# Optimization experiments

Measured on AMD Instinct MI355X. Metric: run time of the kernel, lower is better.

## Reference

```python
import jax, jax.numpy as jnp
import numpy as np

N, E = 50000, 800000
IN_DIM, HID, ZDIM = 256, 128, 64
LN_EPS = 1e-5


def _layernorm(x, gamma, beta):
    mu = jnp.mean(x, axis=-1, keepdims=True)
    var = jnp.mean(jnp.square(x - mu), axis=-1, keepdims=True)
    return (x - mu) * jax.lax.rsqrt(var + LN_EPS) * gamma + beta


def _gcn_conv(h, src, dst, dinv, W, b):
    # h: (N, d_in) -> (N, d_out). GCNConv: X W, then sym-normalized
    # aggregation over edges with self-loops, then bias.
    h = h @ W                                   # (N, d_out)
    coef = dinv[src] * dinv[dst]                # (E,)
    agg = jax.ops.segment_sum(h[src] * coef[:, None], dst,
                              num_segments=h.shape[0])
    agg = agg + h * jnp.square(dinv)[:, None]   # self-loop term
    return agg + b


def setup_inputs() -> dict:
    key = jax.random.key(0)
    ks = jax.random.split(key, 5)
    x = jax.random.normal(ks[0], (N, IN_DIM), dtype=jnp.float32)
    edge_index = jax.random.randint(ks[1], (2, E), 0, N, dtype=jnp.int64)
    s1 = 1.0 / np.sqrt(IN_DIM)
    s2 = 1.0 / np.sqrt(HID)
    return {
        "x": x,
        "edge_index": edge_index,
        "ln_gamma": jnp.ones((IN_DIM,), jnp.float32),
        "ln_beta": jnp.zeros((IN_DIM,), jnp.float32),
        "W1": jax.random.normal(ks[2], (IN_DIM, HID), jnp.float32) * s1,
        "b1": jnp.zeros((HID,), jnp.float32),
        "W2": jax.random.normal(ks[3], (HID, HID), jnp.float32) * s2,
        "b2": jnp.zeros((HID,), jnp.float32),
        "W3": jax.random.normal(ks[4], (HID, ZDIM), jnp.float32) * s2,
        "b3": jnp.zeros((ZDIM,), jnp.float32),
    }


def reference(x, edge_index, ln_gamma, ln_beta, W1, b1, W2, b2, W3, b3):
    src, dst = edge_index[0], edge_index[1]
    n = x.shape[0]
    # degree with self-loops (dropout is inference no-op, training=False)
    deg = jnp.ones((n,), x.dtype).at[dst].add(1.0)
    dinv = jax.lax.rsqrt(deg)
    h = _layernorm(x, ln_gamma, ln_beta)
    h = jax.nn.relu(_gcn_conv(h, src, dst, dinv, W1, b1))
    h = jax.nn.relu(_gcn_conv(h, src, dst, dinv, W2, b2))
    z = _gcn_conv(h, src, dst, dinv, W3, b3)
    return z
```

## Files before the change

kernel.cpp:

```cpp
#include <hip/hip_runtime.h>
#include <cstdint>
#include <cstddef>


typedef __attribute__((ext_vector_type(8))) __bf16 bf16x8;
typedef __attribute__((ext_vector_type(4))) float f32x4;
typedef _Float16 half_t;
typedef __attribute__((ext_vector_type(8))) _Float16 half8_t;

__global__ __launch_bounds__(256) void prep_misc(
    const float* __restrict__ x, const float* __restrict__ W1,
    const float* __restrict__ W2, const float* __restrict__ W3,
    int* __restrict__ bcnt, int* __restrict__ bcur_zero,
    unsigned short* __restrict__ W1t_hi, unsigned short* __restrict__ W1t_lo,
    unsigned short* __restrict__ W2t_hi, unsigned short* __restrict__ W2t_lo,
    unsigned short* __restrict__ W3t_hi, unsigned short* __restrict__ W3t_lo,
    float* __restrict__ mu, float* __restrict__ rs, int n) {
  int blk = blockIdx.x;
  int tid = threadIdx.x;
  if (blk == 0) {
    bcnt[tid] = 0;
    bcur_zero[tid] = 0;
    return;
  }
  if (blk <= 224) {
    int idx = (blk - 1) * 256 + tid;
    const float* W;
    unsigned short *Th, *Tl;
    int K, NOUT;
    if (idx < 32768) {
      W = W1; Th = W1t_hi; Tl = W1t_lo; K = 256; NOUT = 128;
    } else if (idx < 49152) {
      idx -= 32768;
      W = W2; Th = W2t_hi; Tl = W2t_lo; K = 128; NOUT = 128;
    } else {
      idx -= 49152;
      W = W3; Th = W3t_hi; Tl = W3t_lo; K = 128; NOUT = 64;
    }
    int k = idx / NOUT, c = idx % NOUT;
    float v = W[idx];
    __bf16 h = (__bf16)v;
    __bf16 l = (__bf16)(v - (float)h);
    Th[(size_t)c * K + k] = __builtin_bit_cast(unsigned short, h);
    Tl[(size_t)c * K + k] = __builtin_bit_cast(unsigned short, l);
    return;
  }
  int wv = (blk - 225) * 4 + (tid >> 6);
  int lane = tid & 63;
  if (wv >= n) return;
  const float4* row = (const float4*)(x + (size_t)wv * 256);
  float4 v = row[lane];
  float s = v.x + v.y + v.z + v.w;
  float s2 = v.x * v.x + v.y * v.y + v.z * v.z + v.w * v.w;
  for (int off = 32; off > 0; off >>= 1) {
    s += __shfl_down(s, off);
    s2 += __shfl_down(s2, off);
  }
  if (lane == 0) {
    float m = s * (1.0f / 256.0f);
    float var = s2 * (1.0f / 256.0f) - m * m;
    mu[wv] = m;
    rs[wv] = rsqrtf(var + 1e-5f);
  }
}

__global__ __launch_bounds__(256) void hist_bucket(const int* __restrict__ dst,
                                                   int* __restrict__ bcnt, int E, int NB) {
  __shared__ int h[256];
  int t = threadIdx.x;
  h[t] = 0;
  __syncthreads();
  for (int e = blockIdx.x * 256 + t; e < E; e += gridDim.x * 256)
    atomicAdd(&h[dst[e] >> 8], 1);
  __syncthreads();
  if (t < NB && h[t]) atomicAdd(&bcnt[t], h[t]);
}

__global__ __launch_bounds__(256) void scan_buckets(const int* __restrict__ bcnt,
                                                    int* __restrict__ bbase,
                                                    int* __restrict__ bcur, int NB, int E) {
  __shared__ int tmp[256];
  int t = threadIdx.x;
  int v = (t < NB) ? bcnt[t] : 0;
  tmp[t] = v;
  __syncthreads();
  for (int off = 1; off < 256; off <<= 1) {
    int x = (t >= off) ? tmp[t - off] : 0;
    __syncthreads();
    tmp[t] += x;
    __syncthreads();
  }
  int excl = tmp[t] - v;
  if (t < NB) { bbase[t] = excl; bcur[t] = excl; }
  if (t == 0) bbase[NB] = E;
}

#define CHUNK 4096
__global__ __launch_bounds__(256) void scatter_bins(const int* __restrict__ src,
                                                    const int* __restrict__ dst,
                                                    int* __restrict__ bcur,
                                                    unsigned int* __restrict__ binned, int E) {
  __shared__ unsigned int recs[CHUNK];
  __shared__ int hist[256], lbase[256], resv[256], cur[256];
  int t = threadIdx.x;
  int e0 = blockIdx.x * CHUNK;
  if (e0 >= E) return;
  int len = min(CHUNK, E - e0);
  hist[t] = 0;
  cur[t] = 0;
  __syncthreads();
  for (int i = t; i < len; i += 256) atomicAdd(&hist[dst[e0 + i] >> 8], 1);
  __syncthreads();
  int v = hist[t];
  lbase[t] = v;
  __syncthreads();
  for (int off = 1; off < 256; off <<= 1) {
    int x = (t >= off) ? lbase[t - off] : 0;
    __syncthreads();
    lbase[t] += x;
    __syncthreads();
  }
  int myexcl = lbase[t] - v;
  if (v) resv[t] = atomicAdd(&bcur[t], v);
  __syncthreads();
  lbase[t] = myexcl;
  __syncthreads();
  for (int i = t; i < len; i += 256) {
    int d = dst[e0 + i], s = src[e0 + i];
    int b = d >> 8;
    int r = atomicAdd(&cur[b], 1);
    recs[lbase[b] + r] = ((unsigned int)d << 16) | (unsigned int)s;
  }
  __syncthreads();
  for (int i = t; i < len; i += 256) {
    unsigned int rc = recs[i];
    int b = rc >> 24;
    binned[resv[b] + (i - lbase[b])] = rc;
  }
}

#define MAXB 8192
__global__ __launch_bounds__(256) void sort_bucket(const unsigned int* __restrict__ binned,
                                                   const int* __restrict__ bbase,
                                                   int* __restrict__ srcs,
                                                   int* __restrict__ offs,
                                                   float* __restrict__ dinv,
                                                   int N, int NB, int E) {
  __shared__ int sstage[MAXB];
  __shared__ int hist[256], nbase[256], cur[256], tmp[256];
  int b = blockIdx.x, t = threadIdx.x;
  int base = bbase[b], end = bbase[b + 1];
  int L = end - base;
  if (L > MAXB) L = MAXB;
  hist[t] = 0;
  __syncthreads();
  for (int i = t; i < L; i += 256)
    atomicAdd(&hist[(binned[base + i] >> 16) & 255], 1);
  __syncthreads();
  int v = hist[t];
  tmp[t] = v;
  __syncthreads();
  for (int off = 1; off < 256; off <<= 1) {
    int x = (t >= off) ? tmp[t - off] : 0;
    __syncthreads();
    tmp[t] += x;
    __syncthreads();
  }
  int excl = tmp[t] - v;
  nbase[t] = excl;
  cur[t] = excl;
  int node = (b << 8) + t;
  if (node < N) {
    offs[node] = base + excl;
    dinv[node] = rsqrtf(1.0f + (float)v);
  }
  if (b == NB - 1 && t == 0) offs[N] = E;
  __syncthreads();
  for (int i = t; i < L; i += 256) {
    unsigned int p = binned[base + i];
    int ld = (p >> 16) & 255;
    int slot = atomicAdd(&cur[ld], 1);
    sstage[slot] = (int)(p & 0xFFFFu);
  }
  __syncthreads();
  for (int i = t; i < L; i += 256) srcs[base + i] = sstage[i];
}

__global__ void fill_w(const int* __restrict__ srcs, const float* __restrict__ dinv,
                       int2* __restrict__ edges, int E) {
  int e = blockIdx.x * 256 + threadIdx.x;
  if (e < E) {
    int s = srcs[e];
    edges[e] = make_int2(s, __float_as_int(dinv[s]));
  }
}

template <int K, int NOUT, bool LN, bool A_FP16>
__launch_bounds__(256)
__global__ void gemm_mfma(const void* __restrict__ Avoid,
                          const unsigned short* __restrict__ Wt_hi,
                          const unsigned short* __restrict__ Wt_lo,
                          const float* __restrict__ mu, const float* __restrict__ rs,
                          const float* __restrict__ gamma, const float* __restrict__ beta,
                          half_t* __restrict__ out, int nrows) {
  constexpr int BM = 64, BK = 32;
  constexpr int NT = NOUT / 16;
  __shared__ unsigned short As_hi[BM][BK];
  __shared__ unsigned short As_lo[BM][BK];
  __shared__ unsigned short Bs_hi[NOUT][BK];
  __shared__ unsigned short Bs_lo[NOUT][BK];

  const int tid = threadIdx.x;
  const int lane = tid & 63;
  const int w = tid >> 6;
  const int quad = lane >> 4;
  const int l16 = lane & 15;
  const int row0 = blockIdx.x * BM;

  f32x4 acc[NT];
#pragma unroll
  for (int t = 0; t < NT; ++t) acc[t] = (f32x4){0.f, 0.f, 0.f, 0.f};

  for (int k0 = 0; k0 < K; k0 += BK) {
    if (!A_FP16) {
      const float* A = (const float*)Avoid;
#pragma unroll
      for (int i = 0; i < 2; ++i) {
        int r = i * 32 + (tid >> 3);
        int c4 = (tid & 7) * 4;
        int grow = row0 + r;
        if (grow > nrows - 1) grow = nrows - 1;
        float4 v = *(const float4*)&A[(size_t)grow * K + k0 + c4];
        if (LN) {
          float m = mu[grow], s = rs[grow];
          float4 g = *(const float4*)&gamma[k0 + c4];
          float4 b = *(const float4*)&beta[k0 + c4];
          v.x = (v.x - m) * s * g.x + b.x;
          v.y = (v.y - m) * s * g.y + b.y;
          v.z = (v.z - m) * s * g.z + b.z;
          v.w = (v.w - m) * s * g.w + b.w;
        }
        float vv[4] = {v.x, v.y, v.z, v.w};
#pragma unroll
        for (int j = 0; j < 4; ++j) {
          __bf16 h = (__bf16)vv[j];
          __bf16 l = (__bf16)(vv[j] - (float)h);
          As_hi[r][c4 + j] = __builtin_bit_cast(unsigned short, h);
          As_lo[r][c4 + j] = __builtin_bit_cast(unsigned short, l);
        }
      }
    } else {
      const half_t* A = (const half_t*)Avoid;
      int r = tid >> 2;
      int c8 = (tid & 3) * 8;
      int grow = row0 + r;
      if (grow > nrows - 1) grow = nrows - 1;
      half8_t v = *(const half8_t*)&A[(size_t)grow * K + k0 + c8];
#pragma unroll
      for (int j = 0; j < 8; ++j) {
        float f = (float)v[j];
        __bf16 h = (__bf16)f;
        __bf16 l = (__bf16)(f - (float)h);
        As_hi[r][c8 + j] = __builtin_bit_cast(unsigned short, h);
        As_lo[r][c8 + j] = __builtin_bit_cast(unsigned short, l);
      }
    }
#pragma unroll
    for (int i = 0; i < NOUT / 64; ++i) {
      int n = i * 64 + (tid >> 2);
      int c8 = (tid & 3) * 8;
      *(uint4*)&Bs_hi[n][c8] = *(const uint4*)&Wt_hi[(size_t)n * K + k0 + c8];
      *(uint4*)&Bs_lo[n][c8] = *(const uint4*)&Wt_lo[(size_t)n * K + k0 + c8];
    }
    __syncthreads();

    bf16x8 ah = *(const bf16x8*)&As_hi[w * 16 + l16][quad * 8];
    bf16x8 al = *(const bf16x8*)&As_lo[w * 16 + l16][quad * 8];
#pragma unroll
    for (int t = 0; t < NT; ++t) {
      bf16x8 bh = *(const bf16x8*)&Bs_hi[t * 16 + l16][quad * 8];
      bf16x8 bl = *(const bf16x8*)&Bs_lo[t * 16 + l16][quad * 8];
      acc[t] = __builtin_amdgcn_mfma_f32_16x16x32_bf16(ah, bh, acc[t], 0, 0, 0);
      acc[t] = __builtin_amdgcn_mfma_f32_16x16x32_bf16(al, bh, acc[t], 0, 0, 0);
      acc[t] = __builtin_amdgcn_mfma_f32_16x16x32_bf16(ah, bl, acc[t], 0, 0, 0);
    }
    __syncthreads();
  }

#pragma unroll
  for (int t = 0; t < NT; ++t) {
#pragma unroll
    for (int r = 0; r < 4; ++r) {
      int grow = row0 + w * 16 + quad * 4 + r;
      if (grow < nrows) out[(size_t)grow * NOUT + t * 16 + l16] = (half_t)acc[t][r];
    }
  }
}

__global__ __launch_bounds__(256) void agg128_h(const half_t* __restrict__ t,
                                                const int* __restrict__ offs,
                                                const int2* __restrict__ edges,
                                                const float* __restrict__ dinv,
                                                const float* __restrict__ bias,
                                                half_t* __restrict__ out, int n) {
  int gid = blockIdx.x * blockDim.x + threadIdx.x;
  int node = gid >> 6, lane = gid & 63;
  if (node >= n) return;
  int qw = lane >> 4;
  int fl = lane & 15;
  int e0 = offs[node], e1 = offs[node + 1];
  float acc[8] = {0.f, 0.f, 0.f, 0.f, 0.f, 0.f, 0.f, 0.f};
  int e = e0 + qw;
  for (; e + 12 < e1; e += 16) {
    int2 da = edges[e], db = edges[e + 4], dc = edges[e + 8], dd = edges[e + 12];
    half8_t va = *(const half8_t*)(t + ((size_t)da.x << 7) + fl * 8);
    half8_t vb = *(const half8_t*)(t + ((size_t)db.x << 7) + fl * 8);
    half8_t vc = *(const half8_t*)(t + ((size_t)dc.x << 7) + fl * 8);
    half8_t vd = *(const half8_t*)(t + ((size_t)dd.x << 7) + fl * 8);
    float wa = __int_as_float(da.y), wb = __int_as_float(db.y);
    float wc = __int_as_float(dc.y), wd = __int_as_float(dd.y);
#pragma unroll
    for (int j = 0; j < 8; ++j) {
      acc[j] = fmaf(wa, (float)va[j], acc[j]);
      acc[j] = fmaf(wb, (float)vb[j], acc[j]);
      acc[j] = fmaf(wc, (float)vc[j], acc[j]);
      acc[j] = fmaf(wd, (float)vd[j], acc[j]);
    }
  }
  for (; e < e1; e += 4) {
    int2 d = edges[e];
    half8_t v = *(const half8_t*)(t + ((size_t)d.x << 7) + fl * 8);
    float w = __int_as_float(d.y);
#pragma unroll
    for (int j = 0; j < 8; ++j) acc[j] = fmaf(w, (float)v[j], acc[j]);
  }
#pragma unroll
  for (int j = 0; j < 8; ++j) {
    acc[j] += __shfl_xor(acc[j], 16);
    acc[j] += __shfl_xor(acc[j], 32);
  }
  if (qw == 0) {
    float di = dinv[node];
    float dii = di * di;
    half8_t sv = *(const half8_t*)(t + ((size_t)node << 7) + fl * 8);
    float4 b0 = *(const float4*)(bias + fl * 8);
    float4 b1 = *(const float4*)(bias + fl * 8 + 4);
    float bb[8] = {b0.x, b0.y, b0.z, b0.w, b1.x, b1.y, b1.z, b1.w};
    half8_t o;
#pragma unroll
    for (int j = 0; j < 8; ++j) {
      float v = di * acc[j] + dii * (float)sv[j] + bb[j];
      o[j] = (half_t)fmaxf(v, 0.f);
    }
    *(half8_t*)(out + ((size_t)node << 7) + fl * 8) = o;
  }
}

__global__ __launch_bounds__(256) void agg64_h(const half_t* __restrict__ t,
                                               const int* __restrict__ offs,
                                               const int2* __restrict__ edges,
                                               const float* __restrict__ dinv,
                                               const float* __restrict__ bias,
                                               float* __restrict__ out, int n) {
  int gid = blockIdx.x * blockDim.x + threadIdx.x;
  int node = gid >> 6, lane = gid & 63;
  if (node >= n) return;
  int og = lane >> 3;
  int fl = lane & 7;
  int e0 = offs[node], e1 = offs[node + 1];
  float acc[8] = {0.f, 0.f, 0.f, 0.f, 0.f, 0.f, 0.f, 0.f};
  int e = e0 + og;
  for (; e + 8 < e1; e += 16) {
    int2 da = edges[e], db = edges[e + 8];
    half8_t va = *(const half8_t*)(t + ((size_t)da.x << 6) + fl * 8);
    half8_t vb = *(const half8_t*)(t + ((size_t)db.x << 6) + fl * 8);
    float wa = __int_as_float(da.y), wb = __int_as_float(db.y);
#pragma unroll
    for (int j = 0; j < 8; ++j) {
      acc[j] = fmaf(wa, (float)va[j], acc[j]);
      acc[j] = fmaf(wb, (float)vb[j], acc[j]);
    }
  }
  for (; e < e1; e += 8) {
    int2 d = edges[e];
    half8_t v = *(const half8_t*)(t + ((size_t)d.x << 6) + fl * 8);
    float w = __int_as_float(d.y);
#pragma unroll
    for (int j = 0; j < 8; ++j) acc[j] = fmaf(w, (float)v[j], acc[j]);
  }
#pragma unroll
  for (int j = 0; j < 8; ++j) {
    acc[j] += __shfl_xor(acc[j], 8);
    acc[j] += __shfl_xor(acc[j], 16);
    acc[j] += __shfl_xor(acc[j], 32);
  }
  if (og == 0) {
    float di = dinv[node];
    float dii = di * di;
    half8_t sv = *(const half8_t*)(t + ((size_t)node << 6) + fl * 8);
    float4 b0 = *(const float4*)(bias + fl * 8);
    float4 b1 = *(const float4*)(bias + fl * 8 + 4);
    float bb[8] = {b0.x, b0.y, b0.z, b0.w, b1.x, b1.y, b1.z, b1.w};
    float ov[8];
#pragma unroll
    for (int j = 0; j < 8; ++j) ov[j] = di * acc[j] + dii * (float)sv[j] + bb[j];
    *(float4*)(out + ((size_t)node << 6) + fl * 8) = make_float4(ov[0], ov[1], ov[2], ov[3]);
    *(float4*)(out + ((size_t)node << 6) + fl * 8 + 4) = make_float4(ov[4], ov[5], ov[6], ov[7]);
  }
}

extern "C" void kernel_launch(void* const* d_in, const int* in_sizes, int n_in,
                              void* d_out, int out_size, void* d_ws, size_t ws_size,
                              hipStream_t stream) {
  const float* x = (const float*)d_in[0];
  const int* ei = (const int*)d_in[1];
  const float* gamma = (const float*)d_in[2];
  const float* beta = (const float*)d_in[3];
  const float* W1 = (const float*)d_in[4];
  const float* b1 = (const float*)d_in[5];
  const float* W2 = (const float*)d_in[6];
  const float* b2 = (const float*)d_in[7];
  const float* W3 = (const float*)d_in[8];
  const float* b3 = (const float*)d_in[9];
  float* out = (float*)d_out;

  const int N = in_sizes[0] / 256;
  const int E = in_sizes[1] / 2;
  const int* src = ei;
  const int* dst = ei + E;
  const int NB = (N + 255) >> 8;

  char* ws = (char*)d_ws;
  auto alloc = [&](size_t bytes) -> char* {
    char* p = ws;
    ws += (bytes + 255) & ~(size_t)255;
    return p;
  };
  int* bcnt = (int*)alloc(256 * 4);
  int* bbase = (int*)alloc(257 * 4);
  int* bcur = (int*)alloc(256 * 4);
  unsigned int* binned = (unsigned int*)alloc((size_t)E * 4);
  int* srcs = (int*)alloc((size_t)E * 4);
  int* offs = (int*)alloc((size_t)(N + 1) * 4);
  float* dinv = (float*)alloc((size_t)N * 4);
  int2* edges = (int2*)alloc((size_t)E * 8);
  float* mu = (float*)alloc((size_t)N * 4);
  float* rs = (float*)alloc((size_t)N * 4);
  half_t* t = (half_t*)alloc((size_t)N * 128 * 2);
  half_t* h = (half_t*)alloc((size_t)N * 128 * 2);
  unsigned short* W1t_hi = (unsigned short*)alloc(256 * 128 * 2);
  unsigned short* W1t_lo = (unsigned short*)alloc(256 * 128 * 2);
  unsigned short* W2t_hi = (unsigned short*)alloc(128 * 128 * 2);
  unsigned short* W2t_lo = (unsigned short*)alloc(128 * 128 * 2);
  unsigned short* W3t_hi = (unsigned short*)alloc(128 * 64 * 2);
  unsigned short* W3t_lo = (unsigned short*)alloc(128 * 64 * 2);

  const int ln_blocks = (N + 3) / 4;
  prep_misc<<<225 + ln_blocks, 256, 0, stream>>>(
      x, W1, W2, W3, bcnt, bcur, W1t_hi, W1t_lo, W2t_hi, W2t_lo, W3t_hi, W3t_lo,
      mu, rs, N);

  hist_bucket<<<256, 256, 0, stream>>>(dst, bcnt, E, NB);
  scan_buckets<<<1, 256, 0, stream>>>(bcnt, bbase, bcur, NB, E);
  scatter_bins<<<(E + CHUNK - 1) / CHUNK, 256, 0, stream>>>(src, dst, bcur, binned, E);
  sort_bucket<<<NB, 256, 0, stream>>>(binned, bbase, srcs, offs, dinv, N, NB, E);
  fill_w<<<(E + 255) / 256, 256, 0, stream>>>(srcs, dinv, edges, E);

  const int gemm_blocks = (N + 63) / 64;
  const int agg_blocks = (N + 3) / 4;

  gemm_mfma<256, 128, true, false><<<gemm_blocks, 256, 0, stream>>>(
      x, W1t_hi, W1t_lo, mu, rs, gamma, beta, t, N);
  agg128_h<<<agg_blocks, 256, 0, stream>>>(t, offs, edges, dinv, b1, h, N);

  gemm_mfma<128, 128, false, true><<<gemm_blocks, 256, 0, stream>>>(
      h, W2t_hi, W2t_lo, nullptr, nullptr, nullptr, nullptr, t, N);
  agg128_h<<<agg_blocks, 256, 0, stream>>>(t, offs, edges, dinv, b2, h, N);

  gemm_mfma<128, 64, false, true><<<gemm_blocks, 256, 0, stream>>>(
      h, W3t_hi, W3t_lo, nullptr, nullptr, nullptr, nullptr, t, N);
  agg64_h<<<agg_blocks, 256, 0, stream>>>(t, offs, edges, dinv, b3, out, N);
}
```

Measured before the change: 289.9 us.

## Fold dst histogram into prep kernel and drop packed edge-weight array

Moves the bucket histogram into the prep_misc launch as 16 per-slice private histograms that scan_buckets sums, so the separate hist_bucket kernel and its zeroing are gone. It also removes the fill_w kernel and the int2 edges array; the aggregation kernels now read srcs and gather dinv[src] themselves. This cuts two launches and an E-sized write/read pass. In exchange each aggregation does an extra dependent gather of dinv per edge, three times over. The histogram now uses only 16 blocks, which may run slower than the old 256-block version.

```diff
diff --git a/kernel.cpp b/kernel.cpp
--- a/kernel.cpp
+++ b/kernel.cpp
@@ -8,23 +8,34 @@
 typedef _Float16 half_t;
 typedef __attribute__((ext_vector_type(8))) _Float16 half8_t;
 
+#define NHIST 16
+
 __global__ __launch_bounds__(256) void prep_misc(
-    const float* __restrict__ x, const float* __restrict__ W1,
-    const float* __restrict__ W2, const float* __restrict__ W3,
-    int* __restrict__ bcnt, int* __restrict__ bcur_zero,
+    const float* __restrict__ x, const int* __restrict__ dst,
+    const float* __restrict__ W1, const float* __restrict__ W2,
+    const float* __restrict__ W3,
+    int* __restrict__ bcnt_multi,
     unsigned short* __restrict__ W1t_hi, unsigned short* __restrict__ W1t_lo,
     unsigned short* __restrict__ W2t_hi, unsigned short* __restrict__ W2t_lo,
     unsigned short* __restrict__ W3t_hi, unsigned short* __restrict__ W3t_lo,
-    float* __restrict__ mu, float* __restrict__ rs, int n) {
+    float* __restrict__ mu, float* __restrict__ rs, int n, int E) {
   int blk = blockIdx.x;
   int tid = threadIdx.x;
-  if (blk == 0) {
-    bcnt[tid] = 0;
-    bcur_zero[tid] = 0;
+  if (blk < NHIST) {
+    __shared__ int h[256];
+    h[tid] = 0;
+    __syncthreads();
+    int per = (E + NHIST - 1) / NHIST;
+    int lo = blk * per;
+    int hi = lo + per;
+    if (hi > E) hi = E;
+    for (int e = lo + tid; e < hi; e += 256) atomicAdd(&h[dst[e] >> 8], 1);
+    __syncthreads();
+    bcnt_multi[blk * 256 + tid] = h[tid];
     return;
   }
-  if (blk <= 224) {
-    int idx = (blk - 1) * 256 + tid;
+  if (blk < NHIST + 224) {
+    int idx = (blk - NHIST) * 256 + tid;
     const float* W;
     unsigned short *Th, *Tl;
     int K, NOUT;
@@ -45,7 +56,7 @@
     Tl[(size_t)c * K + k] = __builtin_bit_cast(unsigned short, l);
     return;
   }
-  int wv = (blk - 225) * 4 + (tid >> 6);
+  int wv = (blk - (NHIST + 224)) * 4 + (tid >> 6);
   int lane = tid & 63;
   if (wv >= n) return;
   const float4* row = (const float4*)(x + (size_t)wv * 256);
@@ -64,24 +75,14 @@
   }
 }
 
-__global__ __launch_bounds__(256) void hist_bucket(const int* __restrict__ dst,
-                                                   int* __restrict__ bcnt, int E, int NB) {
-  __shared__ int h[256];
-  int t = threadIdx.x;
-  h[t] = 0;
-  __syncthreads();
-  for (int e = blockIdx.x * 256 + t; e < E; e += gridDim.x * 256)
-    atomicAdd(&h[dst[e] >> 8], 1);
-  __syncthreads();
-  if (t < NB && h[t]) atomicAdd(&bcnt[t], h[t]);
-}
-
-__global__ __launch_bounds__(256) void scan_buckets(const int* __restrict__ bcnt,
+__global__ __launch_bounds__(256) void scan_buckets(const int* __restrict__ bcnt_multi,
                                                     int* __restrict__ bbase,
                                                     int* __restrict__ bcur, int NB, int E) {
   __shared__ int tmp[256];
   int t = threadIdx.x;
-  int v = (t < NB) ? bcnt[t] : 0;
+  int v = 0;
+#pragma unroll
+  for (int h = 0; h < NHIST; ++h) v += bcnt_multi[h * 256 + t];
   tmp[t] = v;
   __syncthreads();
   for (int off = 1; off < 256; off <<= 1) {
@@ -184,15 +185,6 @@
   }
   __syncthreads();
   for (int i = t; i < L; i += 256) srcs[base + i] = sstage[i];
-}
-
-__global__ void fill_w(const int* __restrict__ srcs, const float* __restrict__ dinv,
-                       int2* __restrict__ edges, int E) {
-  int e = blockIdx.x * 256 + threadIdx.x;
-  if (e < E) {
-    int s = srcs[e];
-    edges[e] = make_int2(s, __float_as_int(dinv[s]));
-  }
 }
 
 template <int K, int NOUT, bool LN, bool A_FP16>
@@ -299,7 +291,7 @@
 
 __global__ __launch_bounds__(256) void agg128_h(const half_t* __restrict__ t,
                                                 const int* __restrict__ offs,
-                                                const int2* __restrict__ edges,
+                                                const int* __restrict__ srcs,
                                                 const float* __restrict__ dinv,
                                                 const float* __restrict__ bias,
                                                 half_t* __restrict__ out, int n) {
@@ -312,13 +304,12 @@
   float acc[8] = {0.f, 0.f, 0.f, 0.f, 0.f, 0.f, 0.f, 0.f};
   int e = e0 + qw;
   for (; e + 12 < e1; e += 16) {
-    int2 da = edges[e], db = edges[e + 4], dc = edges[e + 8], dd = edges[e + 12];
-    half8_t va = *(const half8_t*)(t + ((size_t)da.x << 7) + fl * 8);
-    half8_t vb = *(const half8_t*)(t + ((size_t)db.x << 7) + fl * 8);
-    half8_t vc = *(const half8_t*)(t + ((size_t)dc.x << 7) + fl * 8);
-    half8_t vd = *(const half8_t*)(t + ((size_t)dd.x << 7) + fl * 8);
-    float wa = __int_as_float(da.y), wb = __int_as_float(db.y);
-    float wc = __int_as_float(dc.y), wd = __int_as_float(dd.y);
+    int sa = srcs[e], sb = srcs[e + 4], sc = srcs[e + 8], sd = srcs[e + 12];
+    float wa = dinv[sa], wb = dinv[sb], wc = dinv[sc], wd = dinv[sd];
+    half8_t va = *(const half8_t*)(t + ((size_t)sa << 7) + fl * 8);
+    half8_t vb = *(const half8_t*)(t + ((size_t)sb << 7) + fl * 8);
+    half8_t vc = *(const half8_t*)(t + ((size_t)sc << 7) + fl * 8);
+    half8_t vd = *(const half8_t*)(t + ((size_t)sd << 7) + fl * 8);
 #pragma unroll
     for (int j = 0; j < 8; ++j) {
       acc[j] = fmaf(wa, (float)va[j], acc[j]);
@@ -328,9 +319,9 @@
     }
   }
   for (; e < e1; e += 4) {
-    int2 d = edges[e];
-    half8_t v = *(const half8_t*)(t + ((size_t)d.x << 7) + fl * 8);
-    float w = __int_as_float(d.y);
+    int s = srcs[e];
+    float w = dinv[s];
+    half8_t v = *(const half8_t*)(t + ((size_t)s << 7) + fl * 8);
 #pragma unroll
     for (int j = 0; j < 8; ++j) acc[j] = fmaf(w, (float)v[j], acc[j]);
   }
@@ -358,7 +349,7 @@
 
 __global__ __launch_bounds__(256) void agg64_h(const half_t* __restrict__ t,
                                                const int* __restrict__ offs,
-                                               const int2* __restrict__ edges,
+                                               const int* __restrict__ srcs,
                                                const float* __restrict__ dinv,
                                                const float* __restrict__ bias,
                                                float* __restrict__ out, int n) {
@@ -371,10 +362,10 @@
   float acc[8] = {0.f, 0.f, 0.f, 0.f, 0.f, 0.f, 0.f, 0.f};
   int e = e0 + og;
   for (; e + 8 < e1; e += 16) {
-    int2 da = edges[e], db = edges[e + 8];
-    half8_t va = *(const half8_t*)(t + ((size_t)da.x << 6) + fl * 8);
-    half8_t vb = *(const half8_t*)(t + ((size_t)db.x << 6) + fl * 8);
-    float wa = __int_as_float(da.y), wb = __int_as_float(db.y);
+    int sa = srcs[e], sb = srcs[e + 8];
+    float wa = dinv[sa], wb = dinv[sb];
+    half8_t va = *(const half8_t*)(t + ((size_t)sa << 6) + fl * 8);
+    half8_t vb = *(const half8_t*)(t + ((size_t)sb << 6) + fl * 8);
 #pragma unroll
     for (int j = 0; j < 8; ++j) {
       acc[j] = fmaf(wa, (float)va[j], acc[j]);
@@ -382,9 +373,9 @@
     }
   }
   for (; e < e1; e += 8) {
-    int2 d = edges[e];
-    half8_t v = *(const half8_t*)(t + ((size_t)d.x << 6) + fl * 8);
-    float w = __int_as_float(d.y);
+    int s = srcs[e];
+    float w = dinv[s];
+    half8_t v = *(const half8_t*)(t + ((size_t)s << 6) + fl * 8);
 #pragma unroll
     for (int j = 0; j < 8; ++j) acc[j] = fmaf(w, (float)v[j], acc[j]);
   }
@@ -436,14 +427,13 @@
     ws += (bytes + 255) & ~(size_t)255;
     return p;
   };
-  int* bcnt = (int*)alloc(256 * 4);
+  int* bcnt_multi = (int*)alloc(NHIST * 256 * 4);
   int* bbase = (int*)alloc(257 * 4);
   int* bcur = (int*)alloc(256 * 4);
   unsigned int* binned = (unsigned int*)alloc((size_t)E * 4);
   int* srcs = (int*)alloc((size_t)E * 4);
   int* offs = (int*)alloc((size_t)(N + 1) * 4);
   float* dinv = (float*)alloc((size_t)N * 4);
-  int2* edges = (int2*)alloc((size_t)E * 8);
   float* mu = (float*)alloc((size_t)N * 4);
   float* rs = (float*)alloc((size_t)N * 4);
   half_t* t = (half_t*)alloc((size_t)N * 128 * 2);
@@ -456,28 +446,26 @@
   unsigned short* W3t_lo = (unsigned short*)alloc(128 * 64 * 2);
 
   const int ln_blocks = (N + 3) / 4;
-  prep_misc<<<225 + ln_blocks, 256, 0, stream>>>(
-      x, W1, W2, W3, bcnt, bcur, W1t_hi, W1t_lo, W2t_hi, W2t_lo, W3t_hi, W3t_lo,
-      mu, rs, N);
-
-  hist_bucket<<<256, 256, 0, stream>>>(dst, bcnt, E, NB);
-  scan_buckets<<<1, 256, 0, stream>>>(bcnt, bbase, bcur, NB, E);
+  prep_misc<<<NHIST + 224 + ln_blocks, 256, 0, stream>>>(
+      x, dst, W1, W2, W3, bcnt_multi, W1t_hi, W1t_lo, W2t_hi, W2t_lo,
+      W3t_hi, W3t_lo, mu, rs, N, E);
+
+  scan_buckets<<<1, 256, 0, stream>>>(bcnt_multi, bbase, bcur, NB, E);
   scatter_bins<<<(E + CHUNK - 1) / CHUNK, 256, 0, stream>>>(src, dst, bcur, binned, E);
   sort_bucket<<<NB, 256, 0, stream>>>(binned, bbase, srcs, offs, dinv, N, NB, E);
-  fill_w<<<(E + 255) / 256, 256, 0, stream>>>(srcs, dinv, edges, E);
 
   const int gemm_blocks = (N + 63) / 64;
   const int agg_blocks = (N + 3) / 4;
 
   gemm_mfma<256, 128, true, false><<<gemm_blocks, 256, 0, stream>>>(
       x, W1t_hi, W1t_lo, mu, rs, gamma, beta, t, N);
-  agg128_h<<<agg_blocks, 256, 0, stream>>>(t, offs, edges, dinv, b1, h, N);
+  agg128_h<<<agg_blocks, 256, 0, stream>>>(t, offs, srcs, dinv, b1, h, N);
 
   gemm_mfma<128, 128, false, true><<<gemm_blocks, 256, 0, stream>>>(
       h, W2t_hi, W2t_lo, nullptr, nullptr, nullptr, nullptr, t, N);
-  agg128_h<<<agg_blocks, 256, 0, stream>>>(t, offs, edges, dinv, b2, h, N);
+  agg128_h<<<agg_blocks, 256, 0, stream>>>(t, offs, srcs, dinv, b2, h, N);
 
   gemm_mfma<128, 64, false, true><<<gemm_blocks, 256, 0, stream>>>(
       h, W3t_hi, W3t_lo, nullptr, nullptr, nullptr, nullptr, t, N);
-  agg64_h<<<agg_blocks, 256, 0, stream>>>(t, offs, edges, dinv, b3, out, N);
-}
+  agg64_h<<<agg_blocks, 256, 0, stream>>>(t, offs, srcs, dinv, b3, out, N);
+}
```

New measurement: 318.7 us. 1.1x slower.
